# Performance work log

Hardware: AMD Instinct MI355X
Metric: run time of the kernel (lower is better)

## Reference

```python
import jax, jax.numpy as jnp
import numpy as np

EPSILON = 1e-19
MASKING_RATIO = 0.75
N_BINS = 64
SIGMA = 0.01


def setup_inputs() -> dict:
    key = jax.random.key(0)
    k1, k2 = jax.random.split(key)
    N, L, D = 4, 512, 1024
    P = 768  # 16*16*3 pixels per patch
    x = jax.random.normal(k1, (N, L, D), dtype=jnp.float32)
    img_pat = jax.random.uniform(k2, (N, L, P), dtype=jnp.float32)
    return {"x": x, "img_pat": img_pat}


def _entropy_kde(values, n_bins=N_BINS, sigma=SIGMA):
    # values: [N, L, P]; global min/max normalization as in the torch code
    bins = jnp.linspace(0.0, 1.0, n_bins, dtype=values.dtype)  # [B]
    vmin = values.min()
    vmax = values.max()
    nv = (values - vmin) / (vmax - vmin)
    # residuals: [N, L, B, P]
    resid = nv[:, :, None, :] - bins[None, None, :, None]
    kern = jnp.exp(-0.5 * (resid / sigma) ** 2)
    pdf = kern.mean(axis=3)  # [N, L, B]
    pdf = pdf / (pdf.sum(axis=2, keepdims=True) + EPSILON) + EPSILON
    return -jnp.sum(pdf * jnp.log(pdf), axis=-1)  # [N, L]


def reference(x, img_pat):
    # entropy_kde_masking branch of MaskingModule.forward
    N, L, D = x.shape
    len_keep = int(L * (1.0 - MASKING_RATIO))
    entropies = _entropy_kde(img_pat)                 # [N, L]
    ids_shuffle = jnp.argsort(entropies, axis=1)      # ascending (descending=False)
    ids_restore = jnp.argsort(ids_shuffle, axis=1)    # [N, L]
    ids_keep = ids_shuffle[:, :len_keep]              # [N, len_keep]
    x_masked = jnp.take_along_axis(x, ids_keep[:, :, None], axis=1)  # [N, len_keep, D]
    mask = jnp.ones((N, L), dtype=x.dtype).at[:, :len_keep].set(0.0)
    mask = jnp.take_along_axis(mask, ids_restore, axis=1)
    return (x_masked, mask, ids_restore)
```

## Files before the change

kernel.cpp:

```cpp
#include <hip/hip_runtime.h>

#define NB 4
#define LB 512
#define DB 1024
#define PB 768
#define NBINS 64
#define LEN_KEEP 128
#define EPSL 1e-19f
#define WIN 4

#if defined(__has_builtin)
#if __has_builtin(__builtin_amdgcn_exp2f)
#define HAVE_EXP2 1
#endif
#endif

__device__ __forceinline__ float fast_exp2(float x) {
#ifdef HAVE_EXP2
    return __builtin_amdgcn_exp2f(x);
#else
    return __expf(x * 0.69314718055994530942f);
#endif
}

__global__ void minmax_partial(const float4* __restrict__ v,
                               float* __restrict__ bmin, float* __restrict__ bmax) {
    __shared__ float smin[256], smax[256];
    int tid = threadIdx.x;
    int base = blockIdx.x * 256 + tid;
    float mn = 1e30f, mx = -1e30f;
#pragma unroll
    for (int k = 0; k < 24; ++k) {
        float4 t4 = v[base + k * 16384];
        mn = fminf(mn, fminf(fminf(t4.x, t4.y), fminf(t4.z, t4.w)));
        mx = fmaxf(mx, fmaxf(fmaxf(t4.x, t4.y), fmaxf(t4.z, t4.w)));
    }
    smin[tid] = mn; smax[tid] = mx;
    __syncthreads();
    for (int s = 128; s > 0; s >>= 1) {
        if (tid < s) {
            smin[tid] = fminf(smin[tid], smin[tid + s]);
            smax[tid] = fmaxf(smax[tid], smax[tid + s]);
        }
        __syncthreads();
    }
    if (tid == 0) { bmin[blockIdx.x] = smin[0]; bmax[blockIdx.x] = smax[0]; }
}

__global__ void entropy_kernel(const float* __restrict__ img,
                               const float* __restrict__ bmin,
                               const float* __restrict__ bmax,
                               float* __restrict__ ent) {
    __shared__ float sh[256];
    __shared__ float snv[PB];
    __shared__ int   cnt[NBINS];
    __shared__ int   bs[NBINS + 1];
    __shared__ int   pos[NBINS];

    int t = blockIdx.x;
    int tid = threadIdx.x;
    int lane = tid & 63;
    int w = tid >> 6;

    if (tid < NBINS) cnt[tid] = 0;
    if (tid < 64) {
        float mn = bmin[tid], mx = bmax[tid];
        for (int m = 1; m < 64; m <<= 1) {
            mn = fminf(mn, __shfl_xor(mn, m, 64));
            mx = fmaxf(mx, __shfl_xor(mx, m, 64));
        }
        if (tid == 0) { sh[0] = mn; sh[1] = mx; }
    }
    __syncthreads();
    float vmin = sh[0], vmax = sh[1];
    float inv = 1.0f / (vmax - vmin);

    const float* row = img + (size_t)t * PB;
    float nv0 = (row[tid]       - vmin) * inv;
    float nv1 = (row[tid + 256] - vmin) * inv;
    float nv2 = (row[tid + 512] - vmin) * inv;
    int m0 = min(63, max(0, __float2int_rn(nv0 * 63.0f)));
    int m1 = min(63, max(0, __float2int_rn(nv1 * 63.0f)));
    int m2 = min(63, max(0, __float2int_rn(nv2 * 63.0f)));
    atomicAdd(&cnt[m0], 1);
    atomicAdd(&cnt[m1], 1);
    atomicAdd(&cnt[m2], 1);
    __syncthreads();

    if (tid < 64) {
        int c = cnt[tid];
        int incl = c;
        for (int off = 1; off < 64; off <<= 1) {
            int up = __shfl_up(incl, off, 64);
            if (tid >= off) incl += up;
        }
        bs[tid + 1] = incl;
        pos[tid] = incl - c;
        if (tid == 0) bs[0] = 0;
    }
    __syncthreads();

    snv[atomicAdd(&pos[m0], 1)] = nv0;
    snv[atomicAdd(&pos[m1], 1)] = nv1;
    snv[atomicAdd(&pos[m2], 1)] = nv2;
    __syncthreads();

    float bv = (float)lane * (1.0f / 63.0f);
    int lo = bs[max(0, lane - WIN)];
    int hi = bs[min(NBINS, lane + WIN + 1)];
    const float negC = -7213.4755859375f;
    float acc = 0.0f;
    for (int j = lo + w; j < hi; j += 4) {
        float d = snv[j] - bv;
        acc += fast_exp2(d * d * negC);
    }
    sh[w * NBINS + lane] = acc;
    __syncthreads();

    if (tid < 64) {
        float pdf = (sh[lane] + sh[64 + lane] + sh[128 + lane] + sh[192 + lane])
                    * (1.0f / (float)PB);
        float s = pdf;
        for (int m = 1; m < 64; m <<= 1) s += __shfl_xor(s, m, 64);
        float p = pdf / (s + EPSL) + EPSL;
        float term = p * __logf(p);
        for (int m = 1; m < 64; m <<= 1) term += __shfl_xor(term, m, 64);
        if (tid == 0) ent[t] = -term;
    }
}

__global__ void rank_kernel(const float* __restrict__ ent,
                            int* __restrict__ ids_keep,
                            float* __restrict__ out_mask,
                            float* __restrict__ out_restore) {
    __shared__ float sh[LB];
    int b = blockIdx.x, tid = threadIdx.x;
    int n = b >> 2;
    int i = (b & 3) * 128 + (tid >> 1);
    int half = tid & 1;

    sh[tid]       = ent[n * LB + tid];
    sh[256 + tid] = ent[n * LB + 256 + tid];
    __syncthreads();

    unsigned long long ci =
        ((unsigned long long)__float_as_uint(sh[i]) << 32) | (unsigned int)i;
    int r = 0;
    int j0 = half * 256;
#pragma unroll 8
    for (int j = j0; j < j0 + 256; ++j) {
        unsigned long long cj =
            ((unsigned long long)__float_as_uint(sh[j]) << 32) | (unsigned int)j;
        r += (cj < ci) ? 1 : 0;
    }
    r += __shfl_xor(r, 1, 64);
    if (half == 0) {
        out_restore[n * LB + i] = (float)r;
        out_mask[n * LB + i] = (r < LEN_KEEP) ? 0.0f : 1.0f;
        if (r < LEN_KEEP) ids_keep[n * LEN_KEEP + r] = i;
    }
}

__global__ void gather_kernel(const float* __restrict__ x,
                              const int* __restrict__ ids_keep,
                              float* __restrict__ out) {
    int i = blockIdx.x;
    int n = blockIdx.y;
    int row = ids_keep[n * LEN_KEEP + i];
    const float4* src = (const float4*)(x + ((size_t)(n * LB + row)) * DB);
    float4* dst = (float4*)(out + ((size_t)(n * LEN_KEEP + i)) * DB);
    dst[threadIdx.x] = src[threadIdx.x];
}

extern "C" void kernel_launch(void* const* d_in, const int* in_sizes, int n_in,
                              void* d_out, int out_size, void* d_ws, size_t ws_size,
                              hipStream_t stream) {
    const float* x   = (const float*)d_in[0];
    const float* img = (const float*)d_in[1];

    float* out      = (float*)d_out;
    float* out_x    = out;
    float* out_mask = out + (size_t)NB * LEN_KEEP * DB;
    float* out_rest = out_mask + NB * LB;

    float* ws   = (float*)d_ws;
    float* bmin = ws;
    float* bmax = ws + 64;
    float* ent  = ws + 128;
    int*   ids  = (int*)(ws + 128 + NB * LB);

    minmax_partial<<<64, 256, 0, stream>>>((const float4*)img, bmin, bmax);
    entropy_kernel<<<NB * LB, 256, 0, stream>>>(img, bmin, bmax, ent);
    rank_kernel<<<16, 256, 0, stream>>>(ent, ids, out_mask, out_rest);
    gather_kernel<<<dim3(LEN_KEEP, NB), 256, 0, stream>>>(x, ids, out_x);
}
```

Baseline: 78.90 us.

## Fuse rank and gather kernels, widen rank parallelism, narrow KDE window

Merges the rank and gather kernels into one launch. Each of 128 blocks ranks 16 rows using 16 threads per row and then copies the kept rows of x directly, which removes one kernel launch and the ids_keep round trip through global memory. It also shrinks the KDE neighbour window from 4 to 3 bins, cutting exp evaluations in the entropy kernel. The narrower window drops kernel contributions at three bin widths, where exp(-0.5*(3/63/0.01)^2) is about 1e-5 relative to the peak. That error could shift entropies slightly and change the ordering of near-tied rows.

```diff
diff --git a/kernel.cpp b/kernel.cpp
--- a/kernel.cpp
+++ b/kernel.cpp
@@ -7,7 +7,7 @@
 #define NBINS 64
 #define LEN_KEEP 128
 #define EPSL 1e-19f
-#define WIN 4
+#define WIN 3
 
 #if defined(__has_builtin)
 #if __has_builtin(__builtin_amdgcn_exp2f)
@@ -129,16 +129,20 @@
     }
 }
 
-__global__ void rank_kernel(const float* __restrict__ ent,
-                            int* __restrict__ ids_keep,
-                            float* __restrict__ out_mask,
-                            float* __restrict__ out_restore) {
+__global__ void rank_gather_kernel(const float* __restrict__ x,
+                                   const float* __restrict__ ent,
+                                   float* __restrict__ out_x,
+                                   float* __restrict__ out_mask,
+                                   float* __restrict__ out_rest) {
     __shared__ float sh[LB];
+    __shared__ int keep_list[16];
+    __shared__ int nkeep;
     int b = blockIdx.x, tid = threadIdx.x;
-    int n = b >> 2;
-    int i = (b & 3) * 128 + (tid >> 1);
-    int half = tid & 1;
-
+    int n = b >> 5;
+    int i = (b & 31) * 16 + (tid >> 4);
+    int slice = tid & 15;
+
+    if (tid == 0) nkeep = 0;
     sh[tid]       = ent[n * LB + tid];
     sh[256 + tid] = ent[n * LB + 256 + tid];
     __syncthreads();
@@ -146,30 +150,36 @@
     unsigned long long ci =
         ((unsigned long long)__float_as_uint(sh[i]) << 32) | (unsigned int)i;
     int r = 0;
-    int j0 = half * 256;
+    int j0 = slice * 32;
 #pragma unroll 8
-    for (int j = j0; j < j0 + 256; ++j) {
+    for (int j = j0; j < j0 + 32; ++j) {
         unsigned long long cj =
             ((unsigned long long)__float_as_uint(sh[j]) << 32) | (unsigned int)j;
         r += (cj < ci) ? 1 : 0;
     }
     r += __shfl_xor(r, 1, 64);
-    if (half == 0) {
-        out_restore[n * LB + i] = (float)r;
+    r += __shfl_xor(r, 2, 64);
+    r += __shfl_xor(r, 4, 64);
+    r += __shfl_xor(r, 8, 64);
+    if (slice == 0) {
+        out_rest[n * LB + i] = (float)r;
         out_mask[n * LB + i] = (r < LEN_KEEP) ? 0.0f : 1.0f;
-        if (r < LEN_KEEP) ids_keep[n * LEN_KEEP + r] = i;
-    }
-}
-
-__global__ void gather_kernel(const float* __restrict__ x,
-                              const int* __restrict__ ids_keep,
-                              float* __restrict__ out) {
-    int i = blockIdx.x;
-    int n = blockIdx.y;
-    int row = ids_keep[n * LEN_KEEP + i];
-    const float4* src = (const float4*)(x + ((size_t)(n * LB + row)) * DB);
-    float4* dst = (float4*)(out + ((size_t)(n * LEN_KEEP + i)) * DB);
-    dst[threadIdx.x] = src[threadIdx.x];
+        if (r < LEN_KEEP) {
+            int e = atomicAdd(&nkeep, 1);
+            keep_list[e] = (r << 16) | i;
+        }
+    }
+    __syncthreads();
+
+    int nk = nkeep;
+    for (int e = 0; e < nk; ++e) {
+        int ent_ri = keep_list[e];
+        int slot = ent_ri >> 16;
+        int rowi = ent_ri & 0xFFFF;
+        const float4* src = (const float4*)(x + ((size_t)(n * LB + rowi)) * DB);
+        float4* dst = (float4*)(out_x + ((size_t)(n * LEN_KEEP + slot)) * DB);
+        dst[tid] = src[tid];
+    }
 }
 
 extern "C" void kernel_launch(void* const* d_in, const int* in_sizes, int n_in,
@@ -187,10 +197,8 @@
     float* bmin = ws;
     float* bmax = ws + 64;
     float* ent  = ws + 128;
-    int*   ids  = (int*)(ws + 128 + NB * LB);
 
     minmax_partial<<<64, 256, 0, stream>>>((const float4*)img, bmin, bmax);
     entropy_kernel<<<NB * LB, 256, 0, stream>>>(img, bmin, bmax, ent);
-    rank_kernel<<<16, 256, 0, stream>>>(ent, ids, out_mask, out_rest);
-    gather_kernel<<<dim3(LEN_KEEP, NB), 256, 0, stream>>>(x, ids, out_x);
-}
+    rank_gather_kernel<<<128, 256, 0, stream>>>(x, ent, out_x, out_mask, out_rest);
+}
```

Result: faster. 75.83 us, median of 2 (-3.9%).
